# Performance work log

Hardware: AMD Instinct MI355X
Metric: run time of the kernel (lower is better)

Reference implementation:

```python
import jax, jax.numpy as jnp
import numpy as np

D_MODEL = 128
D_STATE = 16
KCONV = 3
SQUEEZE = 16
NEIGH = 27
D_INNER = 2 * D_MODEL            # 256
C_CONV = D_INNER // SQUEEZE      # 16 conv3d output channels
D_SEQ = C_CONV * NEIGH           # 432 selective-scan channel dim
DT_RANK = int(np.ceil((D_MODEL // SQUEEZE * NEIGH) / 16))  # 14
LN_EPS = 1e-5


def setup_inputs() -> dict:
    key = jax.random.key(0)
    ks = jax.random.split(key, 10)
    B, Dd, H, W = 2, 16, 16, 16
    x = jax.random.normal(ks[0], (B, Dd, H, W, D_MODEL), dtype=jnp.float32)
    w_in = jax.random.normal(ks[1], (2 * D_INNER, D_MODEL), dtype=jnp.float32) * 0.02
    conv_w = jax.random.normal(ks[2], (C_CONV, SQUEEZE, KCONV, KCONV, KCONV), dtype=jnp.float32) * 0.05
    conv_b = jnp.zeros((C_CONV,), dtype=jnp.float32)
    x_proj_w = jax.random.normal(ks[3], (DT_RANK + 2 * D_STATE, D_SEQ), dtype=jnp.float32) * 0.05
    s = DT_RANK ** -0.5
    dt_w = jax.random.uniform(ks[4], (D_SEQ, DT_RANK), minval=-s, maxval=s, dtype=jnp.float32)
    # dt bias = inverse-softplus of dt ~ LogUniform[1e-3, 0.1]
    dt = jnp.exp(jax.random.uniform(ks[5], (D_SEQ,), dtype=jnp.float32)
                 * (np.log(0.1) - np.log(1e-3)) + np.log(1e-3))
    dt_b = dt + jnp.log(-jnp.expm1(-dt))
    A_logs = jnp.broadcast_to(jnp.log(jnp.arange(1, D_STATE + 1, dtype=jnp.float32)),
                              (D_SEQ, D_STATE)).copy()
    Ds = jnp.ones((D_SEQ,), dtype=jnp.float32)
    w_fold = jax.random.normal(ks[6], (D_INNER, D_SEQ), dtype=jnp.float32) * 0.05
    ln_g = jnp.ones((D_INNER,), dtype=jnp.float32)
    ln_b = jnp.zeros((D_INNER,), dtype=jnp.float32)
    w_out = jax.random.normal(ks[7], (D_MODEL, D_INNER), dtype=jnp.float32) * 0.05
    return dict(x=x, w_in=w_in, conv_w=conv_w, conv_b=conv_b, x_proj_w=x_proj_w,
                dt_w=dt_w, dt_b=dt_b, A_logs=A_logs, Ds=Ds, w_fold=w_fold,
                ln_g=ln_g, ln_b=ln_b, w_out=w_out)


def _selective_scan(u, delta, A, Bm, Cm, Dskip, delta_bias):
    # u, delta: (B, Dch, L); A: (Dch, N); Bm, Cm: (B, N, L); Dskip: (Dch,)
    delta = jax.nn.softplus(delta + delta_bias[None, :, None])
    a = jnp.exp(delta[..., None] * A[None, :, None, :])                     # (B,Dch,L,N)
    b = (delta * u)[..., None] * jnp.swapaxes(Bm, 1, 2)[:, None, :, :]      # (B,Dch,L,N)

    def combine(c1, c2):
        a1, b1 = c1
        a2, b2 = c2
        return a1 * a2, a2 * b1 + b2

    _, h = jax.lax.associative_scan(combine, (a, b), axis=2)                # (B,Dch,L,N)
    y = jnp.einsum('bdln,bnl->bdl', h, Cm)
    return y + Dskip[None, :, None] * u


def _unfold3(x):
    # x: (B, C, D, H, W) -> (B, C*27, D, H, W), channel-major, offset-minor
    B, C, Dd, H, W = x.shape
    p = KCONV // 2
    xp = jnp.pad(x, ((0, 0), (0, 0), (p, p), (p, p), (p, p)))
    taps = jnp.stack([xp[:, :, i:i + Dd, j:j + H, k:k + W]
                      for i in range(KCONV) for j in range(KCONV) for k in range(KCONV)],
                     axis=2)  # (B, C, 27, D, H, W)
    return taps.reshape(B, C * NEIGH, Dd, H, W)


def _forward(x, w_in, conv_w, conv_b, x_proj_w, dt_w, dt_b, A_logs, Ds,
             w_fold, ln_g, ln_b, w_out):
    B, Dd, H, W, _ = x.shape
    L = Dd * H * W
    xz = x @ w_in.T                                   # (B,D,H,W,512)
    xp, z = jnp.split(xz, 2, axis=-1)
    xc = jnp.transpose(xp, (0, 4, 1, 2, 3))           # (B,256,D,H,W)
    xc = jax.lax.conv_general_dilated(
        xc, conv_w, window_strides=(1, 1, 1), padding='SAME',
        dimension_numbers=('NCDHW', 'OIDHW', 'NCDHW'),
        feature_group_count=C_CONV) + conv_b[None, :, None, None, None]
    xc = jax.nn.silu(xc)                              # (B,16,D,H,W)
    xu = _unfold3(xc)                                 # (B,432,D,H,W)
    xs = xu.reshape(B, D_SEQ, L)
    x_dbl = jnp.einsum('bdl,cd->bcl', xs, x_proj_w)   # (B,46,L)
    dts = x_dbl[:, :DT_RANK]
    Bm = x_dbl[:, DT_RANK:DT_RANK + D_STATE]
    Cm = x_dbl[:, DT_RANK + D_STATE:]
    dts = jnp.einsum('brl,dr->bdl', dts, dt_w)        # (B,432,L)
    A = -jnp.exp(A_logs)
    y = _selective_scan(xs, dts, A, Bm, Cm, Ds, dt_b)  # (B,432,L)
    y = jnp.swapaxes(y, 1, 2).reshape(B, Dd, H, W, D_SEQ)
    y = y @ w_fold.T                                   # (B,D,H,W,256)
    mu = jnp.mean(y, axis=-1, keepdims=True)
    var = jnp.var(y, axis=-1, keepdims=True)
    y = (y - mu) * jax.lax.rsqrt(var + LN_EPS) * ln_g + ln_b
    y = y * jax.nn.silu(z)
    return y @ w_out.T                                 # (B,D,H,W,128)


def reference(x, w_in, conv_w, conv_b, x_proj_w, dt_w, dt_b, A_logs, Ds,
              w_fold, ln_g, ln_b, w_out):
    return _forward(x, w_in, conv_w, conv_b, x_proj_w, dt_w, dt_b, A_logs, Ds,
                    w_fold, ln_g, ln_b, w_out)
```

## Files before the change

### kernel.cpp

```cpp
#include <hip/hip_runtime.h>
#include <hip/hip_bf16.h>

#define DM     128
#define DSTATE 16
#define DINNER 256
#define CCONV  16
#define NEIGH  27
#define DSEQ   432
#define DTRANK 14
#define LVOL   4096
#define BATCH  2
#define NTOK   8192

typedef __attribute__((ext_vector_type(8))) unsigned short ushort8_t;
typedef __attribute__((ext_vector_type(8))) short short8_t;
typedef __attribute__((ext_vector_type(4))) float f32x4_t;

__device__ __forceinline__ float bf2f(unsigned short u) {
    union { unsigned int i; float f; } v; v.i = ((unsigned int)u) << 16; return v.f;
}
__device__ __forceinline__ unsigned short f2b(float f) {
    __hip_bfloat16 hb = __float2bfloat16(f);
    return *(unsigned short*)&hb;
}

__global__ void k_wprep(const float* __restrict__ w_in, const float* __restrict__ w_fold,
                        const float* __restrict__ w_out, const float* __restrict__ x_proj_w,
                        unsigned short* __restrict__ wib, unsigned short* __restrict__ wfb,
                        unsigned short* __restrict__ wob, unsigned short* __restrict__ wxpb) {
    int idx = blockIdx.x * 256 + threadIdx.x;
    if (idx < 65536) {
        wib[idx] = f2b(w_in[idx]);
    } else if (idx < 65536 + 114688) {
        int local = idx - 65536;
        int o = local / 448, dk = local - o * 448;
        wfb[local] = (dk < 432) ? f2b(w_fold[o * 432 + dk]) : (unsigned short)0;
    } else if (idx < 65536 + 114688 + 32768) {
        int local = idx - 65536 - 114688;
        wob[local] = f2b(w_out[local]);
    } else if (idx < 65536 + 114688 + 32768 + 21504) {
        int local = idx - 65536 - 114688 - 32768;
        int c = local / 448, dk = local - c * 448;
        wxpb[local] = (c < 46 && dk < 432) ? f2b(x_proj_w[c * 432 + dk]) : (unsigned short)0;
    }
}

__global__ void k_inproj(const float* __restrict__ x, const unsigned short* __restrict__ wib,
                         float* __restrict__ xpt, float* __restrict__ zbufT) {
    int t = threadIdx.x;
    int w = t >> 6, l = t & 63;
    int lc = l & 15, lr = l >> 4;
    int tokbase = blockIdx.x * 32;
    int b = tokbase >> 12, lbase = tokbase & 4095;

    __shared__ unsigned short xsT[32][136];

    for (int idx = t; idx < 1024; idx += 256) {
        int row = idx >> 5, cb = idx & 31;
        float4 v = *(const float4*)(x + (size_t)(tokbase + row) * 128 + cb * 4);
        unsigned int p0 = (unsigned)f2b(v.x) | ((unsigned)f2b(v.y) << 16);
        unsigned int p1 = (unsigned)f2b(v.z) | ((unsigned)f2b(v.w) << 16);
        *(unsigned int*)&xsT[row][cb * 4]     = p0;
        *(unsigned int*)&xsT[row][cb * 4 + 2] = p1;
    }
    __syncthreads();

#pragma unroll
    for (int mi = 0; mi < 8; mi++) {
        int mt = w * 8 + mi;
#pragma unroll
        for (int nt = 0; nt < 2; nt++) {
            f32x4_t acc = (f32x4_t){0.f, 0.f, 0.f, 0.f};
#pragma unroll
            for (int ks = 0; ks < 4; ks++) {
                int kb = ks * 32 + lr * 8;
                short8_t bfr = *(const short8_t*)&xsT[nt * 16 + lc][kb];
                short8_t afr = *(const short8_t*)(wib + (size_t)(mt * 16 + lc) * 128 + kb);
                acc = __builtin_amdgcn_mfma_f32_16x16x32_bf16(afr, bfr, acc, 0, 0, 0);
            }
            int ltok = lbase + nt * 16 + lc;
            int ch = mt * 16 + lr * 4;
            float* dst = (mt < 16)
                ? (xpt   + (size_t)(b * 256 + ch)       * 4096 + ltok)
                : (zbufT + (size_t)(b * 256 + ch - 256) * 4096 + ltok);
#pragma unroll
            for (int r = 0; r < 4; r++)
                dst[(size_t)r * 4096] = acc[r];
        }
    }
}

__global__ void k_conv(const float* __restrict__ xpt, const float* __restrict__ conv_w,
                       const float* __restrict__ conv_b, float* __restrict__ xc) {
    int t = threadIdx.x;
    int tok = blockIdx.x * 256 + t;
    int co = blockIdx.y;
    int b = tok >> 12, l = tok & 4095;
    int d0 = l >> 8, h0 = (l >> 4) & 15, w0 = l & 15;
    int nbo[27];
#pragma unroll
    for (int t27 = 0; t27 < 27; t27++) {
        int di = t27 / 9 - 1, dj = (t27 / 3) % 3 - 1, dk = t27 % 3 - 1;
        int zd = d0 + di, zh = h0 + dj, zw = w0 + dk;
        nbo[t27] = ((unsigned)zd > 15u || (unsigned)zh > 15u || (unsigned)zw > 15u)
                   ? -1 : ((zd << 8) + (zh << 4) + zw);
    }
    const float* xb = xpt + (size_t)(b * 256 + co * 16) * 4096;
    const float* wr = conv_w + co * 432;
    float acc0 = conv_b[co], acc1 = 0.f;
    for (int t27 = 0; t27 < 27; t27++) {
        int o = nbo[t27];
        if (o >= 0) {
#pragma unroll
            for (int q = 0; q < 16; q += 2) {
                acc0 += xb[q * 4096 + o]       * wr[q * 27 + t27];
                acc1 += xb[(q + 1) * 4096 + o] * wr[(q + 1) * 27 + t27];
            }
        }
    }
    float acc = acc0 + acc1;
    acc = acc / (1.f + __expf(-acc));
    xc[(b * 16 + co) * 4096 + l] = acc;
}

__global__ void k_xdbl(const float* __restrict__ xc, const unsigned short* __restrict__ wxpb,
                       float* __restrict__ dts, __hip_bfloat16* __restrict__ bc2) {
    int t = threadIdx.x;
    int w = t >> 6, l = t & 63;
    int lc = l & 15, lr = l >> 4;
    int tokbase = blockIdx.x * 32;
    int b = tokbase >> 12, lbase = tokbase & 4095;

    __shared__ unsigned short xsT[32][456];

    for (int p = t; p < 432; p += 256) {
        int ch = p / 27, tap = p - ch * 27;
        int di = tap / 9 - 1, dj = (tap / 3) % 3 - 1, dk = tap % 3 - 1;
        const float* xr = xc + (size_t)(b * 16 + ch) * 4096;
        for (int tk = 0; tk < 32; tk++) {
            int ll = lbase + tk;
            int zd = (ll >> 8) + di, zh = ((ll >> 4) & 15) + dj, zw = (ll & 15) + dk;
            float v = (((unsigned)zd <= 15u) && ((unsigned)zh <= 15u) && ((unsigned)zw <= 15u))
                      ? xr[(zd << 8) + (zh << 4) + zw] : 0.f;
            xsT[tk][p] = f2b(v);
        }
    }
    for (int idx = t; idx < 16 * 32; idx += 256)
        xsT[idx & 31][432 + (idx >> 5)] = 0;
    __syncthreads();

    for (int ti = w; ti < 6; ti += 4) {
        int mt = ti % 3, nt = ti / 3;
        f32x4_t acc = (f32x4_t){0.f, 0.f, 0.f, 0.f};
        for (int ks = 0; ks < 14; ks++) {
            int kb = ks * 32 + lr * 8;
            short8_t bfr = *(const short8_t*)&xsT[nt * 16 + lc][kb];
            short8_t afr = *(const short8_t*)(wxpb + (size_t)(mt * 16 + lc) * 448 + kb);
            acc = __builtin_amdgcn_mfma_f32_16x16x32_bf16(afr, bfr, acc, 0, 0, 0);
        }
        int ltok = lbase + nt * 16 + lc;
#pragma unroll
        for (int r = 0; r < 4; r++) {
            int c = mt * 16 + lr * 4 + r;
            if (c < 14)
                dts[(size_t)(b * 14 + c) * 4096 + ltok] = acc[r];
            else if (c < 46)
                bc2[(size_t)(b * 32 + (c - 14)) * 4096 + ltok] = __float2bfloat16(acc[r]);
        }
    }
}

__global__ __launch_bounds__(512, 2) void k_scan(
        const float* __restrict__ xc, const float* __restrict__ dts,
        const unsigned short* __restrict__ bc2, const float* __restrict__ dt_w,
        const float* __restrict__ dt_b, const float* __restrict__ A_logs,
        const float* __restrict__ Ds, unsigned short* __restrict__ y) {
    int bd = blockIdx.x;
    int b = bd / 432, dch = bd % 432;
    int t = threadIdx.x;
    int lane = t & 63, wv = t >> 6;

    bool intA = true;
#pragma unroll
    for (int n = 0; n < 16; n++) {
        float An = -__expf(A_logs[dch * 16 + n]);
        intA = intA && (fabsf(An + (float)(n + 1)) < 1e-3f);
    }
    float Dskip = Ds[dch];

    int cch = dch / 27, t27 = dch % 27;
    int di = t27 / 9 - 1, dj = (t27 / 3) % 3 - 1, dk = t27 % 3 - 1;

    float dtv[8];
    {
        float s[8];
        float bias = dt_b[dch];
#pragma unroll
        for (int i = 0; i < 8; i++) s[i] = bias;
        const float* dsb = dts + (size_t)(b * 14) * 4096 + t * 8;
#pragma unroll
        for (int r = 0; r < 14; r++) {
            float d8[8];
            *(float4*)&d8[0] = *(const float4*)(dsb + (size_t)r * 4096);
            *(float4*)&d8[4] = *(const float4*)(dsb + (size_t)r * 4096 + 4);
            float w = dt_w[dch * 14 + r];
#pragma unroll
            for (int i = 0; i < 8; i++) s[i] += d8[i] * w;
        }
#pragma unroll
        for (int i = 0; i < 8; i++)
            dtv[i] = (s[i] > 15.f) ? s[i] : log1pf(__expf(s[i]));
    }

    int d0 = t >> 5, h0 = (t >> 1) & 15, w0 = (t & 1) << 3;
    int zd = d0 + di, zh = h0 + dj;
    bool rowok = ((unsigned)zd <= 15u) && ((unsigned)zh <= 15u);
    const float* xr = xc + (size_t)(b * 16 + cch) * 4096 + (zd << 8) + (zh << 4);
    float dtu[8], ys[8];
#pragma unroll
    for (int i = 0; i < 8; i++) {
        int zw = w0 + i + dk;
        float u = (rowok && (unsigned)zw <= 15u) ? xr[zw] : 0.f;
        dtu[i] = dtv[i] * u;
        ys[i] = Dskip * u;
    }

    const unsigned short* bcb = bc2 + (size_t)(b * 32) * 4096 + t * 8;

    __shared__ float waggA[8][16], waggB[8][16];
    __shared__ float waggS[8];

    float h[16];
    float av[8];

    if (intA) {
        float aw[8];
#pragma unroll
        for (int i = 0; i < 8; i++) { av[i] = __expf(-dtv[i]); aw[i] = av[i]; }
        float sdt = ((dtv[0] + dtv[1]) + (dtv[2] + dtv[3]))
                  + ((dtv[4] + dtv[5]) + (dtv[6] + dtv[7]));

        float Bp[16];
        {
            ushort8_t Bnx = *(const ushort8_t*)(bcb);
#pragma unroll
            for (int n = 0; n < 16; n++) {
                ushort8_t Bv = Bnx;
                if (n < 15) Bnx = *(const ushort8_t*)(bcb + (size_t)(n + 1) * 4096);
                float bp = 0.f;
#pragma unroll
                for (int i = 0; i < 8; i++)
                    bp = aw[i] * bp + dtu[i] * bf2f(Bv[i]);
                Bp[n] = bp;
                if (n < 15) {
#pragma unroll
                    for (int i = 0; i < 8; i++) aw[i] *= av[i];
                }
            }
        }

#pragma unroll
        for (int s = 1; s < 64; s <<= 1) {
            float psdt = __shfl_up(sdt, s, 64);
            float pl = __expf(-sdt);
            float pb[16];
#pragma unroll
            for (int n = 0; n < 16; n++) pb[n] = __shfl_up(Bp[n], s, 64);
            if (lane >= s) {
                float pw = pl;
#pragma unroll
                for (int n = 0; n < 16; n++) {
                    Bp[n] = pw * pb[n] + Bp[n];
                    pw *= pl;
                }
                sdt += psdt;
            }
        }

        if (lane == 63) {
            waggS[wv] = sdt;
#pragma unroll
            for (int n = 0; n < 16; n++) waggB[wv][n] = Bp[n];
        }
        __syncthreads();

        float exsdt = __shfl_up(sdt, 1, 64);
        float exB[16];
#pragma unroll
        for (int n = 0; n < 16; n++) exB[n] = __shfl_up(Bp[n], 1, 64);
        if (lane == 0) {
            exsdt = 0.f;
#pragma unroll
            for (int n = 0; n < 16; n++) exB[n] = 0.f;
        }
        float WB[16];
#pragma unroll
        for (int n = 0; n < 16; n++) WB[n] = 0.f;
        for (int ww = 0; ww < wv; ww++) {
            float plw = __expf(-waggS[ww]);
            float pww = plw;
#pragma unroll
            for (int n = 0; n < 16; n++) {
                WB[n] = pww * WB[n] + waggB[ww][n];
                pww *= plw;
            }
        }
        float pex = __expf(-exsdt);
        float pwx = pex;
#pragma unroll
        for (int n = 0; n < 16; n++) {
            h[n] = pwx * WB[n] + exB[n];
            pwx *= pex;
        }
    } else {
        float A[16];
#pragma unroll
        for (int n = 0; n < 16; n++) A[n] = -__expf(A_logs[dch * 16 + n]);
        float Ap[16], Bp[16];
        ushort8_t Bnx = *(const ushort8_t*)(bcb);
#pragma unroll
        for (int n = 0; n < 16; n++) {
            ushort8_t Bv = Bnx;
            if (n < 15) Bnx = *(const ushort8_t*)(bcb + (size_t)(n + 1) * 4096);
            float ap = 1.f, bp = 0.f, An = A[n];
#pragma unroll
            for (int i = 0; i < 8; i++) {
                float a = __expf(dtv[i] * An);
                bp = a * bp + dtu[i] * bf2f(Bv[i]);
                ap *= a;
            }
            Ap[n] = ap; Bp[n] = bp;
        }
#pragma unroll
        for (int s = 1; s < 64; s <<= 1) {
#pragma unroll
            for (int n = 0; n < 16; n++) {
                float pa = __shfl_up(Ap[n], s, 64);
                float pb = __shfl_up(Bp[n], s, 64);
                if (lane >= s) {
                    Bp[n] = Ap[n] * pb + Bp[n];
                    Ap[n] *= pa;
                }
            }
        }
        if (lane == 63) {
#pragma unroll
            for (int n = 0; n < 16; n++) { waggA[wv][n] = Ap[n]; waggB[wv][n] = Bp[n]; }
        }
        __syncthreads();
#pragma unroll
        for (int n = 0; n < 16; n++) {
            float exA = __shfl_up(Ap[n], 1, 64);
            float exB = __shfl_up(Bp[n], 1, 64);
            if (lane == 0) { exA = 1.f; exB = 0.f; }
            float WB = 0.f;
            for (int ww = 0; ww < wv; ww++)
                WB = waggA[ww][n] * WB + waggB[ww][n];
            h[n] = exA * WB + exB;
        }
    }

    if (intA) {
        float aw[8];
#pragma unroll
        for (int i = 0; i < 8; i++) aw[i] = av[i];
        ushort8_t Bnx = *(const ushort8_t*)(bcb);
        ushort8_t Cnx = *(const ushort8_t*)(bcb + (size_t)16 * 4096);
#pragma unroll
        for (int n = 0; n < 16; n++) {
            ushort8_t Bv = Bnx, Cv = Cnx;
            if (n < 15) {
                Bnx = *(const ushort8_t*)(bcb + (size_t)(n + 1) * 4096);
                Cnx = *(const ushort8_t*)(bcb + (size_t)(17 + n) * 4096);
            }
            float hn = h[n];
#pragma unroll
            for (int i = 0; i < 8; i++) {
                hn = aw[i] * hn + dtu[i] * bf2f(Bv[i]);
                ys[i] += hn * bf2f(Cv[i]);
            }
            if (n < 15) {
#pragma unroll
                for (int i = 0; i < 8; i++) aw[i] *= av[i];
            }
        }
    } else {
        ushort8_t Bnx = *(const ushort8_t*)(bcb);
        ushort8_t Cnx = *(const ushort8_t*)(bcb + (size_t)16 * 4096);
#pragma unroll
        for (int n = 0; n < 16; n++) {
            float An = -__expf(A_logs[dch * 16 + n]);
            ushort8_t Bv = Bnx, Cv = Cnx;
            if (n < 15) {
                Bnx = *(const ushort8_t*)(bcb + (size_t)(n + 1) * 4096);
                Cnx = *(const ushort8_t*)(bcb + (size_t)(17 + n) * 4096);
            }
            float hn = h[n];
#pragma unroll
            for (int i = 0; i < 8; i++) {
                float a = __expf(dtv[i] * An);
                hn = a * hn + dtu[i] * bf2f(Bv[i]);
                ys[i] += hn * bf2f(Cv[i]);
            }
        }
    }

    unsigned short* yo = y + (size_t)(b * 432 + dch) * 4096 + t * 8;
    ushort8_t o8;
#pragma unroll
    for (int i = 0; i < 8; i++) o8[i] = f2b(ys[i]);
    *(ushort8_t*)yo = o8;
}

__global__ void k_tail(const unsigned short* __restrict__ y, const float* __restrict__ zbufT,
                       const unsigned short* __restrict__ wfb, const float* __restrict__ ln_g,
                       const float* __restrict__ ln_b, const unsigned short* __restrict__ wob,
                       float* __restrict__ out) {
    int t = threadIdx.x;
    int w = t >> 6;
    int l = t & 63;
    int lc = l & 15;
    int lr = l >> 4;
    int tokbase = blockIdx.x * 16;
    int b = tokbase >> 12, lbase = tokbase & 4095;

    __shared__ unsigned short Yt[16][456];
    __shared__ unsigned short Pt[16][264];
    __shared__ float red[4][16][2];

    for (int d = t; d < 448; d += 256) {
        if (d < 432) {
            const unsigned short* yr = y + (size_t)(b * 432 + d) * 4096 + lbase;
            ushort8_t v0 = *(const ushort8_t*)(yr);
            ushort8_t v1 = *(const ushort8_t*)(yr + 8);
#pragma unroll
            for (int j = 0; j < 8; j++) { Yt[j][d] = v0[j]; Yt[8 + j][d] = v1[j]; }
        } else {
#pragma unroll
            for (int j = 0; j < 16; j++) Yt[j][d] = 0;
        }
    }
    __syncthreads();

    f32x4_t acc[4];
#pragma unroll
    for (int m = 0; m < 4; m++) acc[m] = (f32x4_t){0.f, 0.f, 0.f, 0.f};
    for (int ks = 0; ks < 14; ks++) {
        int kb = ks * 32 + lr * 8;
        short8_t bf = *(const short8_t*)&Yt[lc][kb];
#pragma unroll
        for (int m = 0; m < 4; m++) {
            int outrow = (4 * w + m) * 16 + lc;
            short8_t af = *(const short8_t*)(wfb + (size_t)outrow * 448 + kb);
            acc[m] = __builtin_amdgcn_mfma_f32_16x16x32_bf16(af, bf, acc[m], 0, 0, 0);
        }
    }

    {
        float s = 0.f, s2 = 0.f;
#pragma unroll
        for (int m = 0; m < 4; m++) {
#pragma unroll
            for (int r = 0; r < 4; r++) { float v = acc[m][r]; s += v; s2 += v * v; }
        }
        s  += __shfl_xor(s, 16, 64);  s2 += __shfl_xor(s2, 16, 64);
        s  += __shfl_xor(s, 32, 64);  s2 += __shfl_xor(s2, 32, 64);
        if (l < 16) { red[w][l][0] = s; red[w][l][1] = s2; }
    }
    __syncthreads();
    float mu, rs;
    {
        float ts  = red[0][lc][0] + red[1][lc][0] + red[2][lc][0] + red[3][lc][0];
        float ts2 = red[0][lc][1] + red[1][lc][1] + red[2][lc][1] + red[3][lc][1];
        mu = ts * (1.f / 256.f);
        float var = ts2 * (1.f / 256.f) - mu * mu;
        rs = rsqrtf(var + 1e-5f);
    }

#pragma unroll
    for (int m = 0; m < 4; m++) {
#pragma unroll
        for (int r = 0; r < 4; r++) {
            int oidx = (4 * w + m) * 16 + lr * 4 + r;
            float g = ln_g[oidx], be = ln_b[oidx];
            float zv = zbufT[(size_t)(b * 256 + oidx) * 4096 + lbase + lc];
            float sz = zv / (1.f + __expf(-zv));
            float p = ((acc[m][r] - mu) * rs * g + be) * sz;
            Pt[lc][oidx] = f2b(p);
        }
    }
    __syncthreads();

    f32x4_t oacc[2];
    oacc[0] = (f32x4_t){0.f, 0.f, 0.f, 0.f};
    oacc[1] = (f32x4_t){0.f, 0.f, 0.f, 0.f};
    for (int ks = 0; ks < 8; ks++) {
        int kb = ks * 32 + lr * 8;
        short8_t bf = *(const short8_t*)&Pt[lc][kb];
#pragma unroll
        for (int m = 0; m < 2; m++) {
            int orow = (2 * w + m) * 16 + lc;
            short8_t af = *(const short8_t*)(wob + (size_t)orow * 256 + kb);
            oacc[m] = __builtin_amdgcn_mfma_f32_16x16x32_bf16(af, bf, oacc[m], 0, 0, 0);
        }
    }
#pragma unroll
    for (int m = 0; m < 2; m++) {
        float o4[4];
#pragma unroll
        for (int r = 0; r < 4; r++) o4[r] = oacc[m][r];
        *(float4*)&out[(size_t)(tokbase + lc) * 128 + (2 * w + m) * 16 + lr * 4] = *(float4*)o4;
    }
}

extern "C" void kernel_launch(void* const* d_in, const int* in_sizes, int n_in,
                              void* d_out, int out_size, void* d_ws, size_t ws_size,
                              hipStream_t stream) {
    const float* x        = (const float*)d_in[0];
    const float* w_in     = (const float*)d_in[1];
    const float* conv_w   = (const float*)d_in[2];
    const float* conv_b   = (const float*)d_in[3];
    const float* x_proj_w = (const float*)d_in[4];
    const float* dt_w     = (const float*)d_in[5];
    const float* dt_b     = (const float*)d_in[6];
    const float* A_logs   = (const float*)d_in[7];
    const float* Ds       = (const float*)d_in[8];
    const float* w_fold   = (const float*)d_in[9];
    const float* ln_g     = (const float*)d_in[10];
    const float* ln_b     = (const float*)d_in[11];
    const float* w_out    = (const float*)d_in[12];
    float* out = (float*)d_out;

    float* ws     = (float*)d_ws;
    float* xpt    = ws;
    float* zbufT  = xpt    + 2097152;
    float* xc     = zbufT  + 2097152;
    float* dts    = xc     + 131072;
    float* bc2    = dts    + 114688;
    float* ybuf   = bc2    + 262144;
    float* wib    = ybuf   + 3538944;
    float* wfb    = wib    + 32768;
    float* wob    = wfb    + 57344;
    float* wxpb   = wob    + 16384;

    k_wprep<<<dim3(916), dim3(256), 0, stream>>>(w_in, w_fold, w_out, x_proj_w,
                                                 (unsigned short*)wib, (unsigned short*)wfb,
                                                 (unsigned short*)wob, (unsigned short*)wxpb);
    k_inproj<<<dim3(NTOK / 32), dim3(256), 0, stream>>>(x, (const unsigned short*)wib,
                                                        xpt, zbufT);
    k_conv<<<dim3(NTOK / 256, CCONV), dim3(256), 0, stream>>>(xpt, conv_w, conv_b, xc);
    k_xdbl<<<dim3(NTOK / 32), dim3(256), 0, stream>>>(xc, (const unsigned short*)wxpb,
                                                      dts, (__hip_bfloat16*)bc2);
    k_scan<<<dim3(BATCH * DSEQ), dim3(512), 0, stream>>>(xc, dts, (const unsigned short*)bc2,
                                                         dt_w, dt_b, A_logs, Ds,
                                                         (unsigned short*)ybuf);
    k_tail<<<dim3(NTOK / 16), dim3(256), 0, stream>>>((const unsigned short*)ybuf, zbufT,
                                                      (const unsigned short*)wfb, ln_g, ln_b,
                                                      (const unsigned short*)wob, out);
}
```

Baseline: 127.3 us.

## Process 16 tokens per thread in scan with 256-thread blocks

Restructures the selective-scan kernel so each thread handles a full 16-element W row serially instead of 8, halving block size to 256 threads and the number of warps taking part in the cross-warp prefix combine. This cuts shuffle-based prefix work and shared-memory aggregation per token. The non-integer-A path now uses exp2f with pre-scaled delta and computes the segment decay product directly from the summed delta. The cost is more registers per thread and a longer serial chain per thread, which may lower occupancy.

```diff
diff --git a/kernel.cpp b/kernel.cpp
--- a/kernel.cpp
+++ b/kernel.cpp
@@ -170,7 +170,7 @@
     }
 }
 
-__global__ __launch_bounds__(512, 2) void k_scan(
+__global__ __launch_bounds__(256, 2) void k_scan(
         const float* __restrict__ xc, const float* __restrict__ dts,
         const unsigned short* __restrict__ bc2, const float* __restrict__ dt_w,
         const float* __restrict__ dt_b, const float* __restrict__ A_logs,
@@ -191,71 +191,80 @@
     int cch = dch / 27, t27 = dch % 27;
     int di = t27 / 9 - 1, dj = (t27 / 3) % 3 - 1, dk = t27 % 3 - 1;
 
-    float dtv[8];
+    float dtv[16];
     {
-        float s[8];
         float bias = dt_b[dch];
 #pragma unroll
-        for (int i = 0; i < 8; i++) s[i] = bias;
-        const float* dsb = dts + (size_t)(b * 14) * 4096 + t * 8;
+        for (int i = 0; i < 16; i++) dtv[i] = bias;
+        const float* dsb = dts + (size_t)(b * 14) * 4096 + t * 16;
 #pragma unroll
         for (int r = 0; r < 14; r++) {
-            float d8[8];
-            *(float4*)&d8[0] = *(const float4*)(dsb + (size_t)r * 4096);
-            *(float4*)&d8[4] = *(const float4*)(dsb + (size_t)r * 4096 + 4);
             float w = dt_w[dch * 14 + r];
-#pragma unroll
-            for (int i = 0; i < 8; i++) s[i] += d8[i] * w;
-        }
-#pragma unroll
-        for (int i = 0; i < 8; i++)
-            dtv[i] = (s[i] > 15.f) ? s[i] : log1pf(__expf(s[i]));
-    }
-
-    int d0 = t >> 5, h0 = (t >> 1) & 15, w0 = (t & 1) << 3;
-    int zd = d0 + di, zh = h0 + dj;
+            const float4* dp = (const float4*)(dsb + (size_t)r * 4096);
+#pragma unroll
+            for (int q = 0; q < 4; q++) {
+                float4 d4 = dp[q];
+                dtv[4 * q + 0] += d4.x * w;
+                dtv[4 * q + 1] += d4.y * w;
+                dtv[4 * q + 2] += d4.z * w;
+                dtv[4 * q + 3] += d4.w * w;
+            }
+        }
+#pragma unroll
+        for (int i = 0; i < 16; i++)
+            dtv[i] = (dtv[i] > 15.f) ? dtv[i] : log1pf(__expf(dtv[i]));
+    }
+
+    int zd = (t >> 4) + di, zh = (t & 15) + dj;
     bool rowok = ((unsigned)zd <= 15u) && ((unsigned)zh <= 15u);
     const float* xr = xc + (size_t)(b * 16 + cch) * 4096 + (zd << 8) + (zh << 4);
-    float dtu[8], ys[8];
-#pragma unroll
-    for (int i = 0; i < 8; i++) {
-        int zw = w0 + i + dk;
+    float dtu[16], ys[16], av[16];
+#pragma unroll
+    for (int i = 0; i < 16; i++) {
+        int zw = i + dk;
         float u = (rowok && (unsigned)zw <= 15u) ? xr[zw] : 0.f;
         dtu[i] = dtv[i] * u;
         ys[i] = Dskip * u;
     }
-
-    const unsigned short* bcb = bc2 + (size_t)(b * 32) * 4096 + t * 8;
-
-    __shared__ float waggA[8][16], waggB[8][16];
-    __shared__ float waggS[8];
+    float sdt = 0.f;
+#pragma unroll
+    for (int i = 0; i < 16; i++) sdt += dtv[i];
+    if (intA) {
+#pragma unroll
+        for (int i = 0; i < 16; i++) av[i] = __expf(-dtv[i]);
+    } else {
+#pragma unroll
+        for (int i = 0; i < 16; i++) av[i] = dtv[i] * 1.44269504f;
+    }
+
+    const unsigned short* bcb = bc2 + (size_t)(b * 32) * 4096 + t * 16;
+
+    __shared__ float waggA[4][16], waggB[4][16];
+    __shared__ float waggS[4];
 
     float h[16];
-    float av[8];
 
     if (intA) {
-        float aw[8];
-#pragma unroll
-        for (int i = 0; i < 8; i++) { av[i] = __expf(-dtv[i]); aw[i] = av[i]; }
-        float sdt = ((dtv[0] + dtv[1]) + (dtv[2] + dtv[3]))
-                  + ((dtv[4] + dtv[5]) + (dtv[6] + dtv[7]));
+        float aw[16];
+#pragma unroll
+        for (int i = 0; i < 16; i++) aw[i] = av[i];
 
         float Bp[16];
-        {
-            ushort8_t Bnx = *(const ushort8_t*)(bcb);
-#pragma unroll
-            for (int n = 0; n < 16; n++) {
-                ushort8_t Bv = Bnx;
-                if (n < 15) Bnx = *(const ushort8_t*)(bcb + (size_t)(n + 1) * 4096);
-                float bp = 0.f;
-#pragma unroll
-                for (int i = 0; i < 8; i++)
-                    bp = aw[i] * bp + dtu[i] * bf2f(Bv[i]);
-                Bp[n] = bp;
-                if (n < 15) {
-#pragma unroll
-                    for (int i = 0; i < 8; i++) aw[i] *= av[i];
-                }
+#pragma unroll
+        for (int n = 0; n < 16; n++) {
+            ushort8_t B0 = *(const ushort8_t*)(bcb + (size_t)n * 4096);
+            ushort8_t B1 = *(const ushort8_t*)(bcb + (size_t)n * 4096 + 8);
+            float bp = 0.f;
+#pragma unroll
+            for (int i = 0; i < 8; i++)
+                bp = aw[i] * bp + dtu[i] * bf2f(B0[i]);
+#pragma unroll
+            for (int i = 8; i < 16; i++)
+                bp = aw[i] * bp + dtu[i] * bf2f(B1[i - 8]);
+            Bp[n] = bp;
+            if (n < 15) {
+#pragma unroll
+                for (int i = 0; i < 16; i++) aw[i] *= av[i];
             }
         }
 
@@ -313,23 +322,26 @@
             pwx *= pex;
         }
     } else {
-        float A[16];
-#pragma unroll
-        for (int n = 0; n < 16; n++) A[n] = -__expf(A_logs[dch * 16 + n]);
         float Ap[16], Bp[16];
-        ushort8_t Bnx = *(const ushort8_t*)(bcb);
+        float s2 = sdt * 1.44269504f;
 #pragma unroll
         for (int n = 0; n < 16; n++) {
-            ushort8_t Bv = Bnx;
-            if (n < 15) Bnx = *(const ushort8_t*)(bcb + (size_t)(n + 1) * 4096);
-            float ap = 1.f, bp = 0.f, An = A[n];
+            float An = -__expf(A_logs[dch * 16 + n]);
+            ushort8_t B0 = *(const ushort8_t*)(bcb + (size_t)n * 4096);
+            ushort8_t B1 = *(const ushort8_t*)(bcb + (size_t)n * 4096 + 8);
+            float bp = 0.f;
 #pragma unroll
             for (int i = 0; i < 8; i++) {
-                float a = __expf(dtv[i] * An);
-                bp = a * bp + dtu[i] * bf2f(Bv[i]);
-                ap *= a;
-            }
-            Ap[n] = ap; Bp[n] = bp;
+                float a = exp2f(av[i] * An);
+                bp = a * bp + dtu[i] * bf2f(B0[i]);
+            }
+#pragma unroll
+            for (int i = 8; i < 16; i++) {
+                float a = exp2f(av[i] * An);
+                bp = a * bp + dtu[i] * bf2f(B1[i - 8]);
+            }
+            Ap[n] = exp2f(s2 * An);
+            Bp[n] = bp;
         }
 #pragma unroll
         for (int s = 1; s < 64; s <<= 1) {
@@ -361,55 +373,61 @@
     }
 
     if (intA) {
-        float aw[8];
-#pragma unroll
-        for (int i = 0; i < 8; i++) aw[i] = av[i];
-        ushort8_t Bnx = *(const ushort8_t*)(bcb);
-        ushort8_t Cnx = *(const ushort8_t*)(bcb + (size_t)16 * 4096);
+        float aw[16];
+#pragma unroll
+        for (int i = 0; i < 16; i++) aw[i] = av[i];
 #pragma unroll
         for (int n = 0; n < 16; n++) {
-            ushort8_t Bv = Bnx, Cv = Cnx;
+            ushort8_t B0 = *(const ushort8_t*)(bcb + (size_t)n * 4096);
+            ushort8_t B1 = *(const ushort8_t*)(bcb + (size_t)n * 4096 + 8);
+            ushort8_t C0 = *(const ushort8_t*)(bcb + (size_t)(16 + n) * 4096);
+            ushort8_t C1 = *(const ushort8_t*)(bcb + (size_t)(16 + n) * 4096 + 8);
+            float hn = h[n];
+#pragma unroll
+            for (int i = 0; i < 8; i++) {
+                hn = aw[i] * hn + dtu[i] * bf2f(B0[i]);
+                ys[i] += hn * bf2f(C0[i]);
+            }
+#pragma unroll
+            for (int i = 8; i < 16; i++) {
+                hn = aw[i] * hn + dtu[i] * bf2f(B1[i - 8]);
+                ys[i] += hn * bf2f(C1[i - 8]);
+            }
             if (n < 15) {
-                Bnx = *(const ushort8_t*)(bcb + (size_t)(n + 1) * 4096);
-                Cnx = *(const ushort8_t*)(bcb + (size_t)(17 + n) * 4096);
-            }
-            float hn = h[n];
-#pragma unroll
-            for (int i = 0; i < 8; i++) {
-                hn = aw[i] * hn + dtu[i] * bf2f(Bv[i]);
-                ys[i] += hn * bf2f(Cv[i]);
-            }
-            if (n < 15) {
-#pragma unroll
-                for (int i = 0; i < 8; i++) aw[i] *= av[i];
+#pragma unroll
+                for (int i = 0; i < 16; i++) aw[i] *= av[i];
             }
         }
     } else {
-        ushort8_t Bnx = *(const ushort8_t*)(bcb);
-        ushort8_t Cnx = *(const ushort8_t*)(bcb + (size_t)16 * 4096);
 #pragma unroll
         for (int n = 0; n < 16; n++) {
             float An = -__expf(A_logs[dch * 16 + n]);
-            ushort8_t Bv = Bnx, Cv = Cnx;
-            if (n < 15) {
-                Bnx = *(const ushort8_t*)(bcb + (size_t)(n + 1) * 4096);
-                Cnx = *(const ushort8_t*)(bcb + (size_t)(17 + n) * 4096);
-            }
+            ushort8_t B0 = *(const ushort8_t*)(bcb + (size_t)n * 4096);
+            ushort8_t B1 = *(const ushort8_t*)(bcb + (size_t)n * 4096 + 8);
+            ushort8_t C0 = *(const ushort8_t*)(bcb + (size_t)(16 + n) * 4096);
+            ushort8_t C1 = *(const ushort8_t*)(bcb + (size_t)(16 + n) * 4096 + 8);
             float hn = h[n];
 #pragma unroll
             for (int i = 0; i < 8; i++) {
-                float a = __expf(dtv[i] * An);
-                hn = a * hn + dtu[i] * bf2f(Bv[i]);
-                ys[i] += hn * bf2f(Cv[i]);
-            }
-        }
-    }
-
-    unsigned short* yo = y + (size_t)(b * 432 + dch) * 4096 + t * 8;
-    ushort8_t o8;
-#pragma unroll
-    for (int i = 0; i < 8; i++) o8[i] = f2b(ys[i]);
-    *(ushort8_t*)yo = o8;
+                float a = exp2f(av[i] * An);
+                hn = a * hn + dtu[i] * bf2f(B0[i]);
+                ys[i] += hn * bf2f(C0[i]);
+            }
+#pragma unroll
+            for (int i = 8; i < 16; i++) {
+                float a = exp2f(av[i] * An);
+                hn = a * hn + dtu[i] * bf2f(B1[i - 8]);
+                ys[i] += hn * bf2f(C1[i - 8]);
+            }
+        }
+    }
+
+    unsigned short* yo = y + (size_t)(b * 432 + dch) * 4096 + t * 16;
+    ushort8_t o0, o1;
+#pragma unroll
+    for (int i = 0; i < 8; i++) { o0[i] = f2b(ys[i]); o1[i] = f2b(ys[8 + i]); }
+    *(ushort8_t*)yo       = o0;
+    *(ushort8_t*)(yo + 8) = o1;
 }
 
 __global__ void k_tail(const unsigned short* __restrict__ y, const float* __restrict__ zbufT,
@@ -551,7 +569,7 @@
     k_conv<<<dim3(NTOK / 256, CCONV), dim3(256), 0, stream>>>(xpt, conv_w, conv_b, xc);
     k_xdbl<<<dim3(NTOK / 32), dim3(256), 0, stream>>>(xc, (const unsigned short*)wxpb,
                                                       dts, (__hip_bfloat16*)bc2);
-    k_scan<<<dim3(BATCH * DSEQ), dim3(512), 0, stream>>>(xc, dts, (const unsigned short*)bc2,
+    k_scan<<<dim3(BATCH * DSEQ), dim3(256), 0, stream>>>(xc, dts, (const unsigned short*)bc2,
                                                          dt_w, dt_b, A_logs, Ds,
                                                          (unsigned short*)ybuf);
     k_tail<<<dim3(NTOK / 16), dim3(256), 0, stream>>>((const unsigned short*)ybuf, zbufT,
```

New measurement: 132.6 us. 1.04x slower.
